# Performance work log

Measured on AMD Instinct MI355X. Metric: run time of the kernel, lower is better.

## Reference

```python
import jax, jax.numpy as jnp
import numpy as np
from jax import lax

B, N, S, NS = 32, 2048, 256, 16   # batch, seeds, proposals (must be 16*16), ball-query samples
C_IN = 256                         # seed_feat_dim
RADIUS = 0.3
EPS = 1e-5
NAB, NVP = 12, 12                  # num_angle_bin, num_viewpoint
GROUPS, PLANES = 4, 64             # SpatialCGNL groups / bottleneck planes
C_OUT = 2 + 3 + 1 + 1 + 2 * NAB + NVP  # 43


def fps(xyz, npoint):
    """Furthest point sampling (torch pointnet2 style: start at index 0)."""
    Bb, Nn, _ = xyz.shape
    def step(carry, _):
        dist, far = carry
        cen = jnp.take_along_axis(xyz, far[:, None, None], axis=1)      # (B,1,3)
        d = jnp.sum((xyz - cen) ** 2, axis=-1)                          # (B,N)
        dist = jnp.minimum(dist, d)
        return (dist, jnp.argmax(dist, axis=1).astype(jnp.int32)), far
    init = (jnp.full((Bb, Nn), 1e10, xyz.dtype), jnp.zeros((Bb,), jnp.int32))
    _, inds = lax.scan(step, init, None, length=npoint)
    return jnp.transpose(inds)  # (B,npoint)


def ball_query(xyz, new_xyz, radius, nsample):
    """First-nsample neighbors within radius; pad by duplicating the first hit."""
    d2 = jnp.sum((new_xyz[:, :, None, :] - xyz[:, None, :, :]) ** 2, axis=-1)  # (B,S,N)
    Nn = xyz.shape[1]
    cand = jnp.where(d2 < radius * radius, jnp.arange(Nn)[None, None, :], Nn)
    idx = jnp.sort(cand, axis=-1)[..., :nsample]
    idx = jnp.where(idx == Nn, idx[..., :1], idx)   # duplicate first hit
    idx = jnp.where(idx == Nn, 0, idx)              # no neighbor at all -> 0
    return idx


def bn1d(x, g, b, m, v):
    """Inference BatchNorm1d over channel axis of (B,C,S)."""
    s = (g * lax.rsqrt(v + EPS))
    return (x - m[None, :, None]) * s[None, :, None] + b[None, :, None]


def forward(xyz, features, sa_w0, sa_w1, sa_w2, sa_gamma, sa_beta, sa_mean, sa_var,
            wt, wp, wg, wz, gn_gamma, gn_beta,
            c1_w, c1_b, bn1_g, bn1_b, bn1_m, bn1_v,
            c2_w, c2_b, bn2_g, bn2_b, bn2_m, bn2_v, c3_w, c3_b):
    # ---- PointnetSAModuleVotes (vote_fps sampling) ----
    fps_inds = fps(xyz, S)                                               # (B,S)
    new_xyz = jnp.take_along_axis(xyz, fps_inds[:, :, None], axis=1)     # (B,S,3)
    idx = ball_query(xyz, new_xyz, RADIUS, NS)                           # (B,S,NS)
    gather = jax.vmap(lambda a, i: a[i])
    g_xyz = (gather(xyz, idx) - new_xyz[:, :, None, :]) / RADIUS         # (B,S,NS,3), normalize_xyz
    g_feat = gather(jnp.transpose(features, (0, 2, 1)), idx)             # (B,S,NS,C)
    h = jnp.concatenate([g_xyz, g_feat], axis=-1)                        # (B,S,NS,3+C)
    for i, w in enumerate((sa_w0, sa_w1, sa_w2)):                        # SharedMLP: conv1x1(no bias)+BN+ReLU
        h = jnp.einsum('bsnc,oc->bsno', h, w)
        h = jax.nn.relu((h - sa_mean[i]) * (sa_gamma[i] * lax.rsqrt(sa_var[i] + EPS)) + sa_beta[i])
    x = jnp.transpose(jnp.max(h, axis=2), (0, 2, 1))                     # max-pool over NS -> (B,128,S)

    # ---- SpatialCGNL (use_scale=False, groups=4), spatial 16x16 flattened to S ----
    t = jnp.einsum('oc,bcn->bon', wt, x)                                 # (B,64,S)
    p = jnp.einsum('oc,bcn->bon', wp, x)
    g = jnp.einsum('oc,bcn->bon', wg, x)
    cg = PLANES // GROUPS                                                # 16
    tg = t.reshape(B, GROUPS, cg * S)
    pg = p.reshape(B, GROUPS, cg * S)
    gg = g.reshape(B, GROUPS, cg * S)
    att = jnp.sum(pg * gg, axis=-1, keepdims=True)                       # (B,G,1) scalar per group
    y = (att * tg).reshape(B, GROUPS, cg, S)                             # (B,G,16,S)
    wz_g = wz.reshape(GROUPS, 128 // GROUPS, cg)                         # grouped 1x1 conv 64->128
    y = jnp.einsum('goc,bgcn->bgon', wz_g, y).reshape(B, 128, S)
    # GroupNorm(num_groups=4, num_channels=128)
    yg = y.reshape(B, GROUPS, -1)
    mu = jnp.mean(yg, axis=-1, keepdims=True)
    var = jnp.mean((yg - mu) ** 2, axis=-1, keepdims=True)
    yn = ((yg - mu) * lax.rsqrt(var + EPS)).reshape(B, 128, S)
    y = yn * gn_gamma[None, :, None] + gn_beta[None, :, None] + x        # affine + residual

    # ---- conv/bn/relu head ----
    h1 = jax.nn.relu(bn1d(jnp.einsum('oc,bcn->bon', c1_w, y) + c1_b[None, :, None], bn1_g, bn1_b, bn1_m, bn1_v))
    h2 = jax.nn.relu(bn1d(jnp.einsum('oc,bcn->bon', c2_w, h1) + c2_b[None, :, None], bn2_g, bn2_b, bn2_m, bn2_v))
    net = jnp.einsum('oc,bcn->bon', c3_w, h2) + c3_b[None, :, None]      # (B,43,S)

    # ---- decode_scores ----
    nt = jnp.transpose(net, (0, 2, 1))                                   # (B,S,43)
    center = new_xyz + nt[:, :, 2:5]
    ang_res_n = nt[:, :, 7 + NAB:7 + 2 * NAB]
    out = jnp.concatenate([
        nt[:, :, 0:2],                    # objectness_scores
        center,                           # center
        nt[:, :, 5:7 + 2 * NAB],          # width, quality, angle_scores, angle_residuals_normalized
        ang_res_n * jnp.float32(np.pi / NAB),  # angle_residuals
        nt[:, :, 7 + 2 * NAB:],           # viewpoint_scores
    ], axis=-1)                           # (B,S,55)
    return out


def setup_inputs():
    key = jax.random.key(0)
    ks = iter(jax.random.split(key, 32))
    rn = lambda shape, s=0.05: jax.random.normal(next(ks), shape, jnp.float32) * s
    return dict(
        xyz=rn((B, N, 3), 1.0),
        features=rn((B, C_IN, N), 1.0),
        sa_w0=rn((128, C_IN + 3)), sa_w1=rn((128, 128)), sa_w2=rn((128, 128)),
        sa_gamma=jnp.ones((3, 128)), sa_beta=jnp.zeros((3, 128)),
        sa_mean=jnp.zeros((3, 128)), sa_var=jnp.ones((3, 128)),
        wt=rn((PLANES, 128)), wp=rn((PLANES, 128)), wg=rn((PLANES, 128)),
        wz=rn((128, PLANES // GROUPS)),
        gn_gamma=jnp.ones((128,)), gn_beta=jnp.zeros((128,)),
        c1_w=rn((128, 128)), c1_b=jnp.zeros((128,)),
        bn1_g=jnp.ones((128,)), bn1_b=jnp.zeros((128,)), bn1_m=jnp.zeros((128,)), bn1_v=jnp.ones((128,)),
        c2_w=rn((128, 128)), c2_b=jnp.zeros((128,)),
        bn2_g=jnp.ones((128,)), bn2_b=jnp.zeros((128,)), bn2_m=jnp.zeros((128,)), bn2_v=jnp.ones((128,)),
        c3_w=rn((C_OUT, 128)), c3_b=jnp.zeros((C_OUT,)),
    )


def reference(xyz, features, sa_w0, sa_w1, sa_w2, sa_gamma, sa_beta, sa_mean, sa_var,
              wt, wp, wg, wz, gn_gamma, gn_beta,
              c1_w, c1_b, bn1_g, bn1_b, bn1_m, bn1_v,
              c2_w, c2_b, bn2_g, bn2_b, bn2_m, bn2_v, c3_w, c3_b):
    return forward(xyz, features, sa_w0, sa_w1, sa_w2, sa_gamma, sa_beta, sa_mean, sa_var,
                   wt, wp, wg, wz, gn_gamma, gn_beta,
                   c1_w, c1_b, bn1_g, bn1_b, bn1_m, bn1_v,
                   c2_w, c2_b, bn2_g, bn2_b, bn2_m, bn2_v, c3_w, c3_b)
```

## Files before the change

### kernel.cpp

```cpp
#include <hip/hip_runtime.h>
#include <hip/hip_bf16.h>
#include <math.h>

#define Bx   32
#define Nx   2048
#define Sx   256
#define NSx  16
#define CINx 256

typedef unsigned short u16;
typedef unsigned int   u32;
typedef unsigned long long u64;
typedef short bf16x8 __attribute__((ext_vector_type(8)));
typedef float f32x4  __attribute__((ext_vector_type(4)));
typedef float f32x16 __attribute__((ext_vector_type(16)));

__device__ __forceinline__ float b2f(u16 u) {
  union { u32 i; float f; } v; v.i = ((u32)u) << 16; return v.f;
}
__device__ __forceinline__ u16 f2b(float x) {
  u32 u = __float_as_uint(x);
  u32 r = (u + 0x7FFFu + ((u >> 16) & 1u)) >> 16;
  return (u16)r;
}
__device__ __forceinline__ float ldin(const void* p, size_t i, int bf) {
  return bf ? b2f(((const u16*)p)[i]) : ((const float*)p)[i];
}

#define DPP_FMAX(x, ctrl)                                                      \
  x = fmaxf(x, __int_as_float(__builtin_amdgcn_update_dpp(                     \
          __float_as_int(x), __float_as_int(x), (ctrl), 0xf, 0xf, false)))

#define OFF_FEATT 0
#define OFF_XT    (33554432)
#define OFF_T     (OFF_XT + 4194304)
#define OFF_YT    (OFF_T + 2097152)
#define OFF_NXYZ  (OFF_YT + 4194304)
#define OFF_IDX   (OFF_NXYZ + 98304)
#define OFF_ATT   (OFF_IDX + 524288)
#define OFF_W0F   (OFF_ATT + 512)
#define OFF_B0    (OFF_W0F + 133120)
#define OFF_W1F   (OFF_B0 + 512)
#define OFF_B1    (OFF_W1F + 65536)
#define OFF_W2F   (OFF_B1 + 512)
#define OFF_B2    (OFF_W2F + 65536)
#define OFF_WTT   (OFF_B2 + 512)
#define OFF_WPT   (OFF_WTT + 32768)
#define OFF_WGT   (OFF_WPT + 32768)
#define OFF_C1T   (OFF_WGT + 32768)
#define OFF_D1    (OFF_C1T + 65536)
#define OFF_C2T   (OFF_D1 + 512)
#define OFF_D2    (OFF_C2T + 65536)
#define OFF_C3T   (OFF_D2 + 512)
#define OFF_WZF   (OFF_C3T + 22016)
#define OFF_GNG   (OFF_WZF + 8192)
#define OFF_GNB   (OFF_GNG + 512)
#define OFF_C3B   (OFF_GNB + 512)
#define OFF_FLAG  (OFF_C3B + 512)

__global__ __launch_bounds__(256) void k_sniff(const u32* __restrict__ w, int* __restrict__ flag) {
  __shared__ int cnt;
  int t = threadIdx.x;
  if (t == 0) cnt = 0;
  __syncthreads();
  u32 x = w[t];
  int e_lo = (x >> 7) & 0xFF;
  if (e_lo >= 100 && e_lo <= 140) atomicAdd(&cnt, 1);
  __syncthreads();
  if (t == 0) *flag = (cnt > 128) ? 1 : 0;
}

#define TRANS_BLKS 4096
__global__ __launch_bounds__(256) void k_mega(
    const void* __restrict__ xyzR, const void* __restrict__ featR,
    const void* sa_w0, const void* sa_w1, const void* sa_w2,
    const void* sa_g,  const void* sa_b,  const void* sa_m, const void* sa_v,
    const void* wt, const void* wp, const void* wg, const void* wzI,
    const void* gngI, const void* gnbI,
    const void* c1w, const void* c1b,
    const void* bn1g, const void* bn1b, const void* bn1m, const void* bn1v,
    const void* c2w, const void* c2b,
    const void* bn2g, const void* bn2b, const void* bn2m, const void* bn2v,
    const void* c3w, const void* c3bI,
    float* __restrict__ nxyz, u16* __restrict__ featT,
    u16* __restrict__ w0F, float* __restrict__ b0, u16* __restrict__ w1F, float* __restrict__ b1,
    u16* __restrict__ w2F, float* __restrict__ b2,
    float* __restrict__ wtT, float* __restrict__ wpT, float* __restrict__ wgT,
    float* __restrict__ c1T, float* __restrict__ d1, float* __restrict__ c2T, float* __restrict__ d2,
    float* __restrict__ c3T, float* __restrict__ wzF, float* __restrict__ gngF,
    float* __restrict__ gnbF, float* __restrict__ c3bF,
    const int* __restrict__ flagp) {
  __shared__ union {
    struct { float sxyz[Nx * 3]; u64 red[2][4]; } fps;
    u16 tile[64][65];
  } sm;
  int bid = blockIdx.x, t = threadIdx.x;
  int bf = *flagp;

  if (bid < Bx) {
    int b = bid;
    const size_t xb = (size_t)b * Nx * 3;
    for (int i = t; i < Nx * 3; i += 256) sm.fps.sxyz[i] = ldin(xyzR, xb + i, bf);
    __syncthreads();
    float px[8], py[8], pz[8], dist[8];
#pragma unroll
    for (int j = 0; j < 8; ++j) {
      int p = t * 8 + j;
      px[j] = sm.fps.sxyz[p * 3 + 0];
      py[j] = sm.fps.sxyz[p * 3 + 1];
      pz[j] = sm.fps.sxyz[p * 3 + 2];
      dist[j] = 1e10f;
    }
    int lane = t & 63, w = t >> 6;
    int far = 0, myind = 0;
    for (int it = 0; it < Sx; ++it) {
      if (t == it) myind = far;
      float cx = sm.fps.sxyz[far * 3 + 0];
      float cy = sm.fps.sxyz[far * 3 + 1];
      float cz = sm.fps.sxyz[far * 3 + 2];
      float bv = -1.f; int bj = 0;
#pragma unroll
      for (int j = 0; j < 8; ++j) {
        float dx = __fsub_rn(px[j], cx);
        float dy = __fsub_rn(py[j], cy);
        float dz = __fsub_rn(pz[j], cz);
        float d = __fadd_rn(__fadd_rn(__fmul_rn(dx, dx), __fmul_rn(dy, dy)), __fmul_rn(dz, dz));
        float nd = fminf(dist[j], d);
        dist[j] = nd;
        if (nd > bv) { bv = nd; bj = j; }
      }
      int bi = t * 8 + bj;
      float x = bv;
      DPP_FMAX(x, 0x111);
      DPP_FMAX(x, 0x112);
      DPP_FMAX(x, 0x114);
      DPP_FMAX(x, 0x118);
      DPP_FMAX(x, 0x142);
      DPP_FMAX(x, 0x143);
      float wmax = __int_as_float(__builtin_amdgcn_readlane(__float_as_int(x), 63));
      u64 mk = __ballot(bv == wmax);
      int srcl = (int)__builtin_ctzll(mk);
      int wbi = __builtin_amdgcn_readlane(bi, srcl);
      if (lane == 63)
        sm.fps.red[it & 1][w] = ((u64)__float_as_uint(wmax) << 32) | (u32)(~wbi);
      __syncthreads();
      u64 k0 = sm.fps.red[it & 1][0], k1 = sm.fps.red[it & 1][1];
      u64 k2 = sm.fps.red[it & 1][2], k3 = sm.fps.red[it & 1][3];
      u64 best = k0 > k1 ? k0 : k1;
      if (k2 > best) best = k2;
      if (k3 > best) best = k3;
      far = (int)(u32)(~(u32)best);
    }
    float* o = nxyz + ((size_t)b * Sx + t) * 3;
    o[0] = sm.fps.sxyz[myind * 3 + 0];
    o[1] = sm.fps.sxyz[myind * 3 + 1];
    o[2] = sm.fps.sxyz[myind * 3 + 2];
  } else if (bid < Bx + TRANS_BLKS) {
    int tb = bid - Bx;
    int nblk = tb & 31, rest = tb >> 5;
    int cblk = rest & 3, b = rest >> 2;
    int n0 = nblk * 64, c0 = cblk * 64;
    int tx = t & 63, ty = t >> 6;
#pragma unroll
    for (int r = ty; r < 64; r += 4) {
      size_t src = ((size_t)(b * CINx + c0 + r)) * Nx + n0 + tx;
      sm.tile[r][tx] = bf ? ((const u16*)featR)[src] : f2b(((const float*)featR)[src]);
    }
    __syncthreads();
#pragma unroll
    for (int r = ty; r < 64; r += 4)
      featT[((size_t)(b * Nx + n0 + r)) * CINx + c0 + tx] = sm.tile[tx][r];
  } else {
    int g0 = (bid - Bx - TRANS_BLKS) * 256 + t;
    const int gs = 64 * 256;
    for (int i = g0; i < 17 * 4 * 64 * 8; i += gs) {
      int j = i & 7, lane = (i >> 3) & 63, nt = (i >> 9) & 3, kt = i >> 11;
      int o = nt * 32 + (lane & 31);
      int c = kt * 16 + ((lane >> 5) << 3) + j;
      float s = ldin(sa_g, o, bf) * rsqrtf(ldin(sa_v, o, bf) + 1e-5f);
      float w;
      if (c < 256) w = ldin(sa_w0, o * 259 + 3 + c, bf);
      else if (c < 259) w = ldin(sa_w0, o * 259 + (c - 256), bf);
      else w = 0.f;
      w0F[i] = f2b(w * s);
    }
    for (int i = g0; i < 8 * 4 * 64 * 8; i += gs) {
      int j = i & 7, lane = (i >> 3) & 63, nt = (i >> 9) & 3, kt = i >> 11;
      int o = nt * 32 + (lane & 31);
      int c = kt * 16 + ((lane >> 5) << 3) + j;
      float s1 = ldin(sa_g, 128 + o, bf) * rsqrtf(ldin(sa_v, 128 + o, bf) + 1e-5f);
      float s2 = ldin(sa_g, 256 + o, bf) * rsqrtf(ldin(sa_v, 256 + o, bf) + 1e-5f);
      w1F[i] = f2b(ldin(sa_w1, o * 128 + c, bf) * s1);
      w2F[i] = f2b(ldin(sa_w2, o * 128 + c, bf) * s2);
    }
    for (int o = g0; o < 128; o += gs) {
      float s0 = ldin(sa_g, o, bf)       * rsqrtf(ldin(sa_v, o, bf)       + 1e-5f);
      float s1 = ldin(sa_g, 128 + o, bf) * rsqrtf(ldin(sa_v, 128 + o, bf) + 1e-5f);
      float s2 = ldin(sa_g, 256 + o, bf) * rsqrtf(ldin(sa_v, 256 + o, bf) + 1e-5f);
      b0[o] = ldin(sa_b, o, bf)       - ldin(sa_m, o, bf)       * s0;
      b1[o] = ldin(sa_b, 128 + o, bf) - ldin(sa_m, 128 + o, bf) * s1;
      b2[o] = ldin(sa_b, 256 + o, bf) - ldin(sa_m, 256 + o, bf) * s2;
      float sc1 = ldin(bn1g, o, bf) * rsqrtf(ldin(bn1v, o, bf) + 1e-5f);
      float sc2 = ldin(bn2g, o, bf) * rsqrtf(ldin(bn2v, o, bf) + 1e-5f);
      d1[o] = (ldin(c1b, o, bf) - ldin(bn1m, o, bf)) * sc1 + ldin(bn1b, o, bf);
      d2[o] = (ldin(c2b, o, bf) - ldin(bn2m, o, bf)) * sc2 + ldin(bn2b, o, bf);
      gngF[o] = ldin(gngI, o, bf);
      gnbF[o] = ldin(gnbI, o, bf);
    }
    for (int i = g0; i < 128 * 128; i += gs) {
      int o = i >> 7, c = i & 127;
      float sc1 = ldin(bn1g, o, bf) * rsqrtf(ldin(bn1v, o, bf) + 1e-5f);
      float sc2 = ldin(bn2g, o, bf) * rsqrtf(ldin(bn2v, o, bf) + 1e-5f);
      c1T[c * 128 + o] = ldin(c1w, i, bf) * sc1;
      c2T[c * 128 + o] = ldin(c2w, i, bf) * sc2;
    }
    for (int i = g0; i < 64 * 128; i += gs) {
      int o = i >> 7, c = i & 127;
      wtT[c * 64 + o] = ldin(wt, i, bf);
      wpT[c * 64 + o] = ldin(wp, i, bf);
      wgT[c * 64 + o] = ldin(wg, i, bf);
    }
    for (int i = g0; i < 43 * 128; i += gs) {
      int o = i >> 7, c = i & 127;
      c3T[c * 43 + o] = ldin(c3w, i, bf);
    }
    for (int i = g0; i < 2048; i += gs) wzF[i] = ldin(wzI, i, bf);
    for (int i = g0; i < 43; i += gs) c3bF[i] = ldin(c3bI, i, bf);
  }
}

__global__ __launch_bounds__(256) void k_fused(
    const u16* __restrict__ featT, const void* __restrict__ xyzR,
    const float* __restrict__ nxyz,
    const u16* __restrict__ w0F, const float* __restrict__ b0v,
    const u16* __restrict__ w1F, const float* __restrict__ b1v,
    const u16* __restrict__ w2F, const float* __restrict__ b2v,
    float* __restrict__ xT, const int* __restrict__ flagp) {
  __shared__ __align__(16) u16 hAa[4][32 * 136];
  __shared__ int ids[4][32];
  int bf = *flagp;
  int t = threadIdx.x, w = t >> 6, lane = t & 63;
  int b = blockIdx.y;
  int s0 = (blockIdx.x * 4 + w) * 2;
  u16* hA = &hAa[w][0];
  int m = lane & 31, half = lane >> 5;
  const size_t xb = (size_t)b * Nx * 3;

  const float* cen0 = nxyz + ((size_t)b * Sx + s0) * 3;
  float c0x = cen0[0], c0y = cen0[1], c0z = cen0[2];
  float c1x = cen0[3], c1y = cen0[4], c1z = cen0[5];

  const float R2 = (float)(0.3 * 0.3);
  u64 below = (lane == 63) ? 0x7fffffffffffffffull : ((1ull << lane) - 1ull);
  int have0 = 0, have1 = 0;
  for (int ch = 0; ch < Nx / 64; ++ch) {
    int p = ch * 64 + lane;
    float px = ldin(xyzR, xb + p * 3 + 0, bf);
    float py = ldin(xyzR, xb + p * 3 + 1, bf);
    float pz = ldin(xyzR, xb + p * 3 + 2, bf);
    float dx0 = __fsub_rn(px, c0x), dy0 = __fsub_rn(py, c0y), dz0 = __fsub_rn(pz, c0z);
    float d0 = __fadd_rn(__fadd_rn(__fmul_rn(dx0, dx0), __fmul_rn(dy0, dy0)), __fmul_rn(dz0, dz0));
    float dx1 = __fsub_rn(px, c1x), dy1 = __fsub_rn(py, c1y), dz1 = __fsub_rn(pz, c1z);
    float d1 = __fadd_rn(__fadd_rn(__fmul_rn(dx1, dx1), __fmul_rn(dy1, dy1)), __fmul_rn(dz1, dz1));
    bool h0 = d0 < R2, h1 = d1 < R2;
    u64 m0 = __ballot(h0), m1 = __ballot(h1);
    if (h0) { int pos = have0 + __popcll(m0 & below); if (pos < NSx) ids[w][pos] = p; }
    if (h1) { int pos = have1 + __popcll(m1 & below); if (pos < NSx) ids[w][16 + pos] = p; }
    have0 += __popcll(m0);
    have1 += __popcll(m1);
  }
  if (lane < 32) {
    int c = lane >> 4, i = lane & 15;
    int hv = c ? have1 : have0;
    if (i >= hv && i < NSx) ids[w][c * 16 + i] = ids[w][c * 16];
  }
  int pn = ids[w][m];

  float rcx = half ? c1x : c0x, rcy = half ? c1y : c0y, rcz = half ? c1z : c0z;
  float pcx = (m >> 4) ? c1x : c0x, pcy = (m >> 4) ? c1y : c0y, pcz = (m >> 4) ? c1z : c0z;
  (void)rcx; (void)rcy; (void)rcz;
  bf16x8 a_tail = (bf16x8)(short)0;
  {
    float gx = ldin(xyzR, xb + (size_t)pn * 3 + 0, bf);
    float gy = ldin(xyzR, xb + (size_t)pn * 3 + 1, bf);
    float gz = ldin(xyzR, xb + (size_t)pn * 3 + 2, bf);
    if (half == 0) {
      a_tail[0] = (short)f2b((gx - pcx) * (1.0f / 0.3f));
      a_tail[1] = (short)f2b((gy - pcy) * (1.0f / 0.3f));
      a_tail[2] = (short)f2b((gz - pcz) * (1.0f / 0.3f));
    }
  }

  const bf16x8* wf0 = (const bf16x8*)w0F;
  const bf16x8* wf1 = (const bf16x8*)w1F;
  const bf16x8* wf2 = (const bf16x8*)w2F;
  f32x16 acc[4];

#pragma unroll
  for (int nt = 0; nt < 4; ++nt) acc[nt] = (f32x16)(0.f);
  const u16* arow = featT + ((size_t)b * Nx + pn) * CINx + half * 8;
#pragma unroll
  for (int kt = 0; kt < 17; ++kt) {
    bf16x8 a = (kt < 16) ? *(const bf16x8*)(arow + kt * 16) : a_tail;
#pragma unroll
    for (int nt = 0; nt < 4; ++nt)
      acc[nt] = __builtin_amdgcn_mfma_f32_32x32x16_bf16(a, wf0[(kt * 4 + nt) * 64 + lane], acc[nt], 0, 0, 0);
  }
#pragma unroll
  for (int nt = 0; nt < 4; ++nt) {
    float bb = b0v[nt * 32 + m];
#pragma unroll
    for (int r = 0; r < 16; ++r) {
      int mm = (r & 3) + 8 * (r >> 2) + 4 * half;
      hA[mm * 136 + nt * 32 + m] = f2b(fmaxf(acc[nt][r] + bb, 0.f));
    }
  }
#pragma unroll
  for (int nt = 0; nt < 4; ++nt) acc[nt] = (f32x16)(0.f);
#pragma unroll
  for (int kt = 0; kt < 8; ++kt) {
    bf16x8 a = *(const bf16x8*)(hA + m * 136 + kt * 16 + half * 8);
#pragma unroll
    for (int nt = 0; nt < 4; ++nt)
      acc[nt] = __builtin_amdgcn_mfma_f32_32x32x16_bf16(a, wf1[(kt * 4 + nt) * 64 + lane], acc[nt], 0, 0, 0);
  }
#pragma unroll
  for (int nt = 0; nt < 4; ++nt) {
    float bb = b1v[nt * 32 + m];
#pragma unroll
    for (int r = 0; r < 16; ++r) {
      int mm = (r & 3) + 8 * (r >> 2) + 4 * half;
      hA[mm * 136 + nt * 32 + m] = f2b(fmaxf(acc[nt][r] + bb, 0.f));
    }
  }
#pragma unroll
  for (int nt = 0; nt < 4; ++nt) acc[nt] = (f32x16)(0.f);
#pragma unroll
  for (int kt = 0; kt < 8; ++kt) {
    bf16x8 a = *(const bf16x8*)(hA + m * 136 + kt * 16 + half * 8);
#pragma unroll
    for (int nt = 0; nt < 4; ++nt)
      acc[nt] = __builtin_amdgcn_mfma_f32_32x32x16_bf16(a, wf2[(kt * 4 + nt) * 64 + lane], acc[nt], 0, 0, 0);
  }
#pragma unroll
  for (int nt = 0; nt < 4; ++nt) {
    float v0 = acc[nt][0], v1 = acc[nt][8];
#pragma unroll
    for (int r = 1; r < 8; ++r) { v0 = fmaxf(v0, acc[nt][r]); v1 = fmaxf(v1, acc[nt][8 + r]); }
    v0 = fmaxf(v0, __shfl_xor(v0, 32, 64));
    v1 = fmaxf(v1, __shfl_xor(v1, 32, 64));
    int o = nt * 32 + m;
    float vv = half ? v1 : v0;
    xT[((size_t)b * Sx + s0 + half) * 128 + o] = fmaxf(vv + b2v[o], 0.f);
  }
}

__device__ __forceinline__ float blocksum(float v, volatile float* red, int t) {
#pragma unroll
  for (int off = 32; off; off >>= 1) v += __shfl_down(v, off, 64);
  __syncthreads();
  if ((t & 63) == 0) red[t >> 6] = v;
  __syncthreads();
  return red[0] + red[1] + red[2] + red[3];
}

__global__ __launch_bounds__(256) void k_tpgn(const float* __restrict__ xT,
                                              const float* __restrict__ wtT,
                                              const float* __restrict__ wpT,
                                              const float* __restrict__ wgT,
                                              const float* __restrict__ wzF,
                                              const float* __restrict__ gngF,
                                              const float* __restrict__ gnbF,
                                              float* __restrict__ yT) {
  __shared__ float xs[64][129];
  __shared__ float tS[16][260];
  __shared__ float wts[3][128][16];
  __shared__ float wzs[32][16];
  __shared__ float red[4];
  int g = blockIdx.x, b = blockIdx.y, t = threadIdx.x;
  for (int i = t; i < 512; i += 256)
    wzs[i >> 4][i & 15] = wzF[(g * 32 + (i >> 4)) * 16 + (i & 15)];
  for (int i = t; i < 128 * 16; i += 256) {
    int c = i >> 4, r2 = i & 15;
    wts[0][c][r2] = wtT[c * 64 + g * 16 + r2];
    wts[1][c][r2] = wpT[c * 64 + g * 16 + r2];
    wts[2][c][r2] = wgT[c * 64 + g * 16 + r2];
  }
  int r = t >> 4, sg = t & 15;
  float attp = 0.f;
  for (int tile = 0; tile < 4; ++tile) {
    {
      int rr = t >> 2, part = (t & 3) * 32;
      const float4* src = (const float4*)(xT + ((size_t)b * Sx + tile * 64 + rr) * 128 + part);
#pragma unroll
      for (int q = 0; q < 8; ++q) {
        float4 v = src[q];
        xs[rr][part + q * 4 + 0] = v.x;
        xs[rr][part + q * 4 + 1] = v.y;
        xs[rr][part + q * 4 + 2] = v.z;
        xs[rr][part + q * 4 + 3] = v.w;
      }
    }
    __syncthreads();
    float ta[4], pa[4], ga[4];
#pragma unroll
    for (int j = 0; j < 4; ++j) { ta[j] = 0.f; pa[j] = 0.f; ga[j] = 0.f; }
    for (int c = 0; c < 128; ++c) {
      float wa = wts[0][c][r];
      float wb = wts[1][c][r];
      float wc = wts[2][c][r];
#pragma unroll
      for (int j = 0; j < 4; ++j) {
        float xv = xs[sg * 4 + j][c];
        ta[j] = fmaf(wa, xv, ta[j]);
        pa[j] = fmaf(wb, xv, pa[j]);
        ga[j] = fmaf(wc, xv, ga[j]);
      }
    }
#pragma unroll
    for (int j = 0; j < 4; ++j) {
      attp += pa[j] * ga[j];
      tS[r][tile * 64 + sg * 4 + j] = ta[j];
    }
    __syncthreads();
  }
  float attv = blocksum(attp, red, t);
  int s = t;
  float yv[32];
#pragma unroll
  for (int o = 0; o < 32; ++o) yv[o] = 0.f;
  for (int c = 0; c < 16; ++c) {
    float tv = attv * tS[c][s];
#pragma unroll
    for (int o = 0; o < 32; ++o) yv[o] = fmaf(wzs[o][c], tv, yv[o]);
  }
  float ls = 0.f;
#pragma unroll
  for (int o = 0; o < 32; ++o) ls += yv[o];
  float mu = blocksum(ls, red, t) * (1.f / 8192.f);
  float lq = 0.f;
#pragma unroll
  for (int o = 0; o < 32; ++o) { float d = yv[o] - mu; lq = fmaf(d, d, lq); }
  float var = blocksum(lq, red, t) * (1.f / 8192.f);
  float rs = rsqrtf(var + 1e-5f);
  const float* xrow = xT + ((size_t)b * Sx + s) * 128 + g * 32;
  float* yrow = yT + ((size_t)b * Sx + s) * 128 + g * 32;
#pragma unroll
  for (int o = 0; o < 32; ++o) {
    int ch = g * 32 + o;
    yrow[o] = (yv[o] - mu) * rs * gngF[ch] + gnbF[ch] + xrow[o];
  }
}

__global__ __launch_bounds__(256) void k_ffn(const float* __restrict__ yT,
                                             const float* __restrict__ c1T, const float* __restrict__ d1,
                                             const float* __restrict__ c2T, const float* __restrict__ d2,
                                             const float* __restrict__ c3T, const float* __restrict__ c3bF,
                                             const float* __restrict__ nxyz,
                                             void* __restrict__ outp,
                                             const int* __restrict__ flagp) {
  __shared__ float ys[32][132];
  __shared__ float h1s[32][132];
  __shared__ float h2s[32][132];
  __shared__ float nets[32][44];
  int bf = *flagp;
  int b = blockIdx.y, s0 = blockIdx.x * 32, t = threadIdx.x;
  {
    int r = t >> 3, part = (t & 7) * 16;
    const float4* src = (const float4*)(yT + ((size_t)b * Sx + s0 + r) * 128 + part);
#pragma unroll
    for (int q = 0; q < 4; ++q) *(float4*)&ys[r][part + q * 4] = src[q];
  }
  __syncthreads();
  int o0 = (t & 31) * 4, sl0 = (t >> 5) * 4;
  float acc[16];
#pragma unroll
  for (int k = 0; k < 16; ++k) acc[k] = 0.f;
  for (int c = 0; c < 128; ++c) {
    float4 wv = *(const float4*)(c1T + c * 128 + o0);
    float yv[4];
#pragma unroll
    for (int j = 0; j < 4; ++j) yv[j] = ys[sl0 + j][c];
#pragma unroll
    for (int j = 0; j < 4; ++j) {
      acc[0 * 4 + j] = fmaf(wv.x, yv[j], acc[0 * 4 + j]);
      acc[1 * 4 + j] = fmaf(wv.y, yv[j], acc[1 * 4 + j]);
      acc[2 * 4 + j] = fmaf(wv.z, yv[j], acc[2 * 4 + j]);
      acc[3 * 4 + j] = fmaf(wv.w, yv[j], acc[3 * 4 + j]);
    }
  }
  {
    float4 dv = *(const float4*)(d1 + o0);
    float db[4] = {dv.x, dv.y, dv.z, dv.w};
#pragma unroll
    for (int i = 0; i < 4; ++i)
#pragma unroll
      for (int j = 0; j < 4; ++j)
        h1s[sl0 + j][o0 + i] = fmaxf(acc[i * 4 + j] + db[i], 0.f);
  }
  __syncthreads();
#pragma unroll
  for (int k = 0; k < 16; ++k) acc[k] = 0.f;
  for (int c = 0; c < 128; ++c) {
    float4 wv = *(const float4*)(c2T + c * 128 + o0);
    float yv[4];
#pragma unroll
    for (int j = 0; j < 4; ++j) yv[j] = h1s[sl0 + j][c];
#pragma unroll
    for (int j = 0; j < 4; ++j) {
      acc[0 * 4 + j] = fmaf(wv.x, yv[j], acc[0 * 4 + j]);
      acc[1 * 4 + j] = fmaf(wv.y, yv[j], acc[1 * 4 + j]);
      acc[2 * 4 + j] = fmaf(wv.z, yv[j], acc[2 * 4 + j]);
      acc[3 * 4 + j] = fmaf(wv.w, yv[j], acc[3 * 4 + j]);
    }
  }
  {
    float4 dv = *(const float4*)(d2 + o0);
    float db[4] = {dv.x, dv.y, dv.z, dv.w};
#pragma unroll
    for (int i = 0; i < 4; ++i)
#pragma unroll
      for (int j = 0; j < 4; ++j)
        h2s[sl0 + j][o0 + i] = fmaxf(acc[i * 4 + j] + db[i], 0.f);
  }
  __syncthreads();
  for (int f = t; f < 43 * 32; f += 256) {
    int o = f >> 5, s = f & 31;
    float a = c3bF[o];
    for (int c4 = 0; c4 < 32; ++c4) {
      float4 hv = *(const float4*)&h2s[s][c4 * 4];
      a = fmaf(hv.x, c3T[(c4 * 4 + 0) * 43 + o], a);
      a = fmaf(hv.y, c3T[(c4 * 4 + 1) * 43 + o], a);
      a = fmaf(hv.z, c3T[(c4 * 4 + 2) * 43 + o], a);
      a = fmaf(hv.w, c3T[(c4 * 4 + 3) * 43 + o], a);
    }
    nets[s][o] = a;
  }
  __syncthreads();
  const float PI12 = (float)(M_PI / 12.0);
  for (int f = t; f < 55 * 32; f += 256) {
    int s = f / 55, kk = f - s * 55;
    float v;
    if (kk < 5) {
      v = nets[s][kk];
      if (kk >= 2) v += nxyz[((size_t)b * Sx + s0 + s) * 3 + (kk - 2)];
    } else if (kk < 31) v = nets[s][kk];
    else if (kk < 43) v = nets[s][kk - 12] * PI12;
    else v = nets[s][kk - 12];
    size_t oi = ((size_t)b * Sx + s0 + s) * 55 + kk;
    if (bf) ((u16*)outp)[oi] = f2b(v);
    else    ((float*)outp)[oi] = v;
  }
}

extern "C" void kernel_launch(void* const* d_in, const int* in_sizes, int n_in,
                              void* d_out, int out_size, void* d_ws, size_t ws_size,
                              hipStream_t stream) {
  char* w = (char*)d_ws;
  u16*   featT = (u16*)(w + OFF_FEATT);
  float* xT    = (float*)(w + OFF_XT);
  float* yT    = (float*)(w + OFF_YT);
  float* nxyz  = (float*)(w + OFF_NXYZ);
  u16*   w0F   = (u16*)(w + OFF_W0F);
  float* b0    = (float*)(w + OFF_B0);
  u16*   w1F   = (u16*)(w + OFF_W1F);
  float* b1    = (float*)(w + OFF_B1);
  u16*   w2F   = (u16*)(w + OFF_W2F);
  float* b2    = (float*)(w + OFF_B2);
  float* wtT   = (float*)(w + OFF_WTT);
  float* wpT   = (float*)(w + OFF_WPT);
  float* wgT   = (float*)(w + OFF_WGT);
  float* c1T   = (float*)(w + OFF_C1T);
  float* d1    = (float*)(w + OFF_D1);
  float* c2T   = (float*)(w + OFF_C2T);
  float* d2    = (float*)(w + OFF_D2);
  float* c3T   = (float*)(w + OFF_C3T);
  float* wzF   = (float*)(w + OFF_WZF);
  float* gngF  = (float*)(w + OFF_GNG);
  float* gnbF  = (float*)(w + OFF_GNB);
  float* c3bF  = (float*)(w + OFF_C3B);
  int*   flag  = (int*)(w + OFF_FLAG);

  k_sniff<<<1, 256, 0, stream>>>((const u32*)d_in[0], flag);
  k_mega<<<Bx + TRANS_BLKS + 64, 256, 0, stream>>>(
      d_in[0], d_in[1],
      d_in[2], d_in[3], d_in[4], d_in[5], d_in[6], d_in[7], d_in[8],
      d_in[9], d_in[10], d_in[11], d_in[12], d_in[13], d_in[14],
      d_in[15], d_in[16], d_in[17], d_in[18], d_in[19], d_in[20],
      d_in[21], d_in[22], d_in[23], d_in[24], d_in[25], d_in[26],
      d_in[27], d_in[28],
      nxyz, featT,
      w0F, b0, w1F, b1, w2F, b2, wtT, wpT, wgT,
      c1T, d1, c2T, d2, c3T, wzF, gngF, gnbF, c3bF, flag);
  k_fused<<<dim3(Sx / 8, Bx), 256, 0, stream>>>(featT, d_in[0], nxyz,
                                                w0F, b0, w1F, b1, w2F, b2, xT, flag);
  k_tpgn<<<dim3(4, Bx), 256, 0, stream>>>(xT, wtT, wpT, wgT, wzF, gngF, gnbF, yT);
  k_ffn<<<dim3(8, Bx), 256, 0, stream>>>(yT, c1T, d1, c2T, d2, c3T, c3bF, nxyz,
                                         d_out, flag);
}
```

Measured before the change: 433.9 us.

## Inline dtype sniff per kernel and carry FPS centroid coords through reduction

Removes the separate single-block sniff kernel launch. Each kernel now detects bf16 vs fp32 input with a per-wave ballot over the first 64 words of xyz. The FPS loop also carries the winning point's coordinates through the cross-wave reduction, so the next centroid no longer needs a dependent LDS lookup by index. This drops one launch and shortens the serial FPS iteration, at the cost of redundant sniff loads in every block and a slightly larger reduction record.

New measurement: 490.4 us. 13.0% more time.

```diff
diff --git a/kernel.cpp b/kernel.cpp
--- a/kernel.cpp
+++ b/kernel.cpp
@@ -25,6 +25,13 @@
 }
 __device__ __forceinline__ float ldin(const void* p, size_t i, int bf) {
   return bf ? b2f(((const u16*)p)[i]) : ((const float*)p)[i];
+}
+
+__device__ __forceinline__ int sniff_bf(const void* xyzR) {
+  u32 x = ((const u32*)xyzR)[threadIdx.x & 63];
+  int e = (x >> 7) & 0xFF;
+  u64 m = __ballot(e >= 100 && e <= 140);
+  return __popcll(m) >= 48;
 }
 
 #define DPP_FMAX(x, ctrl)                                                      \
@@ -56,19 +63,6 @@
 #define OFF_GNG   (OFF_WZF + 8192)
 #define OFF_GNB   (OFF_GNG + 512)
 #define OFF_C3B   (OFF_GNB + 512)
-#define OFF_FLAG  (OFF_C3B + 512)
-
-__global__ __launch_bounds__(256) void k_sniff(const u32* __restrict__ w, int* __restrict__ flag) {
-  __shared__ int cnt;
-  int t = threadIdx.x;
-  if (t == 0) cnt = 0;
-  __syncthreads();
-  u32 x = w[t];
-  int e_lo = (x >> 7) & 0xFF;
-  if (e_lo >= 100 && e_lo <= 140) atomicAdd(&cnt, 1);
-  __syncthreads();
-  if (t == 0) *flag = (cnt > 128) ? 1 : 0;
-}
 
 #define TRANS_BLKS 4096
 __global__ __launch_bounds__(256) void k_mega(
@@ -88,14 +82,13 @@
     float* __restrict__ wtT, float* __restrict__ wpT, float* __restrict__ wgT,
     float* __restrict__ c1T, float* __restrict__ d1, float* __restrict__ c2T, float* __restrict__ d2,
     float* __restrict__ c3T, float* __restrict__ wzF, float* __restrict__ gngF,
-    float* __restrict__ gnbF, float* __restrict__ c3bF,
-    const int* __restrict__ flagp) {
+    float* __restrict__ gnbF, float* __restrict__ c3bF) {
   __shared__ union {
-    struct { float sxyz[Nx * 3]; u64 red[2][4]; } fps;
+    struct { float sxyz[Nx * 3]; float rec[2][4][8]; } fps;
     u16 tile[64][65];
   } sm;
   int bid = blockIdx.x, t = threadIdx.x;
-  int bf = *flagp;
+  int bf = sniff_bf(xyzR);
 
   if (bid < Bx) {
     int b = bid;
@@ -113,23 +106,21 @@
     }
     int lane = t & 63, w = t >> 6;
     int far = 0, myind = 0;
+    float fcx = sm.fps.sxyz[0], fcy = sm.fps.sxyz[1], fcz = sm.fps.sxyz[2];
     for (int it = 0; it < Sx; ++it) {
       if (t == it) myind = far;
-      float cx = sm.fps.sxyz[far * 3 + 0];
-      float cy = sm.fps.sxyz[far * 3 + 1];
-      float cz = sm.fps.sxyz[far * 3 + 2];
-      float bv = -1.f; int bj = 0;
+      float bv = -1.f; int bi = 0;
+      float bx = 0.f, by = 0.f, bz = 0.f;
 #pragma unroll
       for (int j = 0; j < 8; ++j) {
-        float dx = __fsub_rn(px[j], cx);
-        float dy = __fsub_rn(py[j], cy);
-        float dz = __fsub_rn(pz[j], cz);
+        float dx = __fsub_rn(px[j], fcx);
+        float dy = __fsub_rn(py[j], fcy);
+        float dz = __fsub_rn(pz[j], fcz);
         float d = __fadd_rn(__fadd_rn(__fmul_rn(dx, dx), __fmul_rn(dy, dy)), __fmul_rn(dz, dz));
         float nd = fminf(dist[j], d);
         dist[j] = nd;
-        if (nd > bv) { bv = nd; bj = j; }
+        if (nd > bv) { bv = nd; bi = t * 8 + j; bx = px[j]; by = py[j]; bz = pz[j]; }
       }
-      int bi = t * 8 + bj;
       float x = bv;
       DPP_FMAX(x, 0x111);
       DPP_FMAX(x, 0x112);
@@ -140,16 +131,28 @@
       float wmax = __int_as_float(__builtin_amdgcn_readlane(__float_as_int(x), 63));
       u64 mk = __ballot(bv == wmax);
       int srcl = (int)__builtin_ctzll(mk);
-      int wbi = __builtin_amdgcn_readlane(bi, srcl);
-      if (lane == 63)
-        sm.fps.red[it & 1][w] = ((u64)__float_as_uint(wmax) << 32) | (u32)(~wbi);
+      int p = it & 1;
+      if (lane == srcl) {
+        float4 r4;
+        r4.x = bv;
+        r4.y = __uint_as_float((u32)bi);
+        r4.z = bx; r4.w = by;
+        *(float4*)&sm.fps.rec[p][w][0] = r4;
+        sm.fps.rec[p][w][4] = bz;
+      }
       __syncthreads();
-      u64 k0 = sm.fps.red[it & 1][0], k1 = sm.fps.red[it & 1][1];
-      u64 k2 = sm.fps.red[it & 1][2], k3 = sm.fps.red[it & 1][3];
-      u64 best = k0 > k1 ? k0 : k1;
-      if (k2 > best) best = k2;
-      if (k3 > best) best = k3;
-      far = (int)(u32)(~(u32)best);
+      float4 r0 = *(const float4*)&sm.fps.rec[p][0][0]; float z0 = sm.fps.rec[p][0][4];
+      float4 r1 = *(const float4*)&sm.fps.rec[p][1][0]; float z1 = sm.fps.rec[p][1][4];
+      float4 r2 = *(const float4*)&sm.fps.rec[p][2][0]; float z2 = sm.fps.rec[p][2][4];
+      float4 r3 = *(const float4*)&sm.fps.rec[p][3][0]; float z3 = sm.fps.rec[p][3][4];
+      bool s01 = (r1.x > r0.x) || (r1.x == r0.x && __float_as_uint(r1.y) < __float_as_uint(r0.y));
+      float4 ra = s01 ? r1 : r0; float za = s01 ? z1 : z0;
+      bool s23 = (r3.x > r2.x) || (r3.x == r2.x && __float_as_uint(r3.y) < __float_as_uint(r2.y));
+      float4 rb = s23 ? r3 : r2; float zb = s23 ? z3 : z2;
+      bool sab = (rb.x > ra.x) || (rb.x == ra.x && __float_as_uint(rb.y) < __float_as_uint(ra.y));
+      float4 rf = sab ? rb : ra; float zf = sab ? zb : za;
+      far = (int)__float_as_uint(rf.y);
+      fcx = rf.z; fcy = rf.w; fcz = zf;
     }
     float* o = nxyz + ((size_t)b * Sx + t) * 3;
     o[0] = sm.fps.sxyz[myind * 3 + 0];
@@ -235,10 +238,10 @@
     const u16* __restrict__ w0F, const float* __restrict__ b0v,
     const u16* __restrict__ w1F, const float* __restrict__ b1v,
     const u16* __restrict__ w2F, const float* __restrict__ b2v,
-    float* __restrict__ xT, const int* __restrict__ flagp) {
+    float* __restrict__ xT) {
   __shared__ __align__(16) u16 hAa[4][32 * 136];
   __shared__ int ids[4][32];
-  int bf = *flagp;
+  int bf = sniff_bf(xyzR);
   int t = threadIdx.x, w = t >> 6, lane = t & 63;
   int b = blockIdx.y;
   int s0 = (blockIdx.x * 4 + w) * 2;
@@ -276,9 +279,7 @@
   }
   int pn = ids[w][m];
 
-  float rcx = half ? c1x : c0x, rcy = half ? c1y : c0y, rcz = half ? c1z : c0z;
   float pcx = (m >> 4) ? c1x : c0x, pcy = (m >> 4) ? c1y : c0y, pcz = (m >> 4) ? c1z : c0z;
-  (void)rcx; (void)rcy; (void)rcz;
   bf16x8 a_tail = (bf16x8)(short)0;
   {
     float gx = ldin(xyzR, xb + (size_t)pn * 3 + 0, bf);
@@ -457,13 +458,13 @@
                                              const float* __restrict__ c2T, const float* __restrict__ d2,
                                              const float* __restrict__ c3T, const float* __restrict__ c3bF,
                                              const float* __restrict__ nxyz,
-                                             void* __restrict__ outp,
-                                             const int* __restrict__ flagp) {
+                                             const void* __restrict__ xyzR,
+                                             void* __restrict__ outp) {
   __shared__ float ys[32][132];
   __shared__ float h1s[32][132];
   __shared__ float h2s[32][132];
   __shared__ float nets[32][44];
-  int bf = *flagp;
+  int bf = sniff_bf(xyzR);
   int b = blockIdx.y, s0 = blockIdx.x * 32, t = threadIdx.x;
   {
     int r = t >> 3, part = (t & 7) * 16;
@@ -579,9 +580,7 @@
   float* gngF  = (float*)(w + OFF_GNG);
   float* gnbF  = (float*)(w + OFF_GNB);
   float* c3bF  = (float*)(w + OFF_C3B);
-  int*   flag  = (int*)(w + OFF_FLAG);
-
-  k_sniff<<<1, 256, 0, stream>>>((const u32*)d_in[0], flag);
+
   k_mega<<<Bx + TRANS_BLKS + 64, 256, 0, stream>>>(
       d_in[0], d_in[1],
       d_in[2], d_in[3], d_in[4], d_in[5], d_in[6], d_in[7], d_in[8],
@@ -591,10 +590,10 @@
       d_in[27], d_in[28],
       nxyz, featT,
       w0F, b0, w1F, b1, w2F, b2, wtT, wpT, wgT,
-      c1T, d1, c2T, d2, c3T, wzF, gngF, gnbF, c3bF, flag);
+      c1T, d1, c2T, d2, c3T, wzF, gngF, gnbF, c3bF);
   k_fused<<<dim3(Sx / 8, Bx), 256, 0, stream>>>(featT, d_in[0], nxyz,
-                                                w0F, b0, w1F, b1, w2F, b2, xT, flag);
+                                                w0F, b0, w1F, b1, w2F, b2, xT);
   k_tpgn<<<dim3(4, Bx), 256, 0, stream>>>(xT, wtT, wpT, wgT, wzF, gngF, gnbF, yT);
   k_ffn<<<dim3(8, Bx), 256, 0, stream>>>(yT, c1T, d1, c2T, d2, c3T, c3bF, nxyz,
-                                         d_out, flag);
-}
+                                         d_in[0], d_out);
+}
```
